# Performance work log

Hardware: AMD Instinct MI355X
Metric: run time of the kernel (lower is better)

Reference implementation:

```python
import jax, jax.numpy as jnp
import numpy as np

B, C, P, H, W, S = 4, 256, 128, 56, 56, 5
EPS = 1e-5


def setup_inputs() -> dict:
    key = jax.random.key(0)
    ks = jax.random.split(key, 6)
    return {
        "x": jax.random.normal(ks[0], (B, C, H, W), jnp.float32),
        "Wt": jax.random.normal(ks[1], (P, C), jnp.float32) * 0.05,
        "Wp": jax.random.normal(ks[2], (P, C), jnp.float32) * 0.05,
        "Wg": jax.random.normal(ks[3], (S, P, C), jnp.float32) * 0.05,
        "W1": jax.random.normal(ks[4], (S, C, P), jnp.float32) * 0.05,
        "W2": jax.random.normal(ks[5], (S, C, P), jnp.float32) * 0.05,
        "gamma": jnp.ones((S, C), jnp.float32),
        "beta": jnp.zeros((S, C), jnp.float32),
    }


def _batchnorm(o, g, b):
    # training-mode BN over (batch, spatial); o: [b, C, n]
    mean = o.mean(axis=(0, 2), keepdims=True)
    var = ((o - mean) ** 2).mean(axis=(0, 2), keepdims=True)
    return (o - mean) * jax.lax.rsqrt(var + EPS) * g[None, :, None] + b[None, :, None]


def reference(x, Wt, Wp, Wg, W1, W2, gamma, beta):
    b, c, h, w = x.shape
    n = h * w
    xf = x.reshape(b, c, n)
    # 1x1 conv projections == channel matmuls
    t = jax.nn.relu(jnp.einsum('pc,bcn->bpn', Wt, xf))  # is_norm branch uses relu
    p = jax.nn.relu(jnp.einsum('pc,bcn->bpn', Wp, xf))
    att = jnp.einsum('bpi,bpj->bij', t, p)              # [b, n, n] affinity
    att = 0.5 * (att + jnp.swapaxes(att, 1, 2))         # is_sys symmetrization
    d = att.sum(axis=2)                                  # degree [b, n]
    d_safe = jnp.where(d != 0, d, 1.0)
    d_inv = jnp.where(d != 0, jax.lax.rsqrt(d_safe), 0.0)
    att = att * d_inv[:, None, :] * d_inv[:, :, None]    # D^-1/2 A D^-1/2
    out = xf
    for s in range(S):  # fixed small stage count
        g = jnp.einsum('pc,bcn->bpn', Wg[s], out)        # [b, P, n]
        ag = jnp.einsum('bij,bpj->bpi', att, g)          # att @ g over spatial
        o = jnp.einsum('cp,bpn->bcn', W1[s], ag) + jnp.einsum('cp,bpn->bcn', W2[s], g)
        out = _batchnorm(o, gamma[s], beta[s]) + out     # BN + residual
    return out.reshape(b, c, h, w)
```

## Files before the change

kernel.cpp:

```cpp
#include <hip/hip_runtime.h>

namespace {

constexpr int Bc = 4;
constexpr int Cc = 256;
constexpr int Pc = 128;
constexpr int NcT = 3136;
constexpr int Np = 3200;
constexpr int Sc = 5;
constexpr int KSn = 5;
constexpr int KCH = 640;
constexpr float EPSc = 1e-5f;

typedef __attribute__((ext_vector_type(8))) short bf16x8;
typedef __attribute__((ext_vector_type(4))) float f32x4;
typedef __attribute__((ext_vector_type(8))) unsigned short u16x8;
typedef __attribute__((ext_vector_type(4))) unsigned short u16x4;

__device__ inline float bf2f(unsigned short u) {
    return __uint_as_float(((unsigned)u) << 16);
}
__device__ inline unsigned short f2bf(float f) {
    unsigned u = __float_as_uint(f);
    return (unsigned short)((u + 0x7FFFu + ((u >> 16) & 1u)) >> 16);
}

struct GP {
    const unsigned short* A; int lda; long aB; long aSl;
    const unsigned short* Bw; int ldb; long bB; long bSl;
    const unsigned short* A2; int lda2; long aB2;
    const unsigned short* B2; int ldb2; long bB2;
    int K; int K2; int nsl; int kchunk;
    unsigned short* outSM; int ldsm; long smB; long smSlice;
    unsigned short* outCM; long cmB;
    float* ps; float* ps2;
    const float* dinv;
    const unsigned short* oin; const float* bnsc; const float* bnsh;
    float* resid;
};

template <int MT, int EPI, int CMOUT, bool SPLITK, int BNSTAT, bool FUSEBN,
          bool XORM, bool DUALK>
__global__ __launch_bounds__(256) void mgemm(GP p)
{
    constexpr int TBA = MT * 64 * 2;
    constexpr int TBB = 128 * 64 * 2;
    constexpr int BUF = TBA + TBB;
    constexpr int OTB = MT * 132 * 4;
    constexpr int LDSZ = (2 * BUF > OTB + 2048) ? 2 * BUF : (OTB + 2048);
    __shared__ __align__(16) char lds[LDSZ];

    int b, kstart;
    long smOff;
    if (SPLITK) {
        b = blockIdx.z & 3;
        int ks = blockIdx.z >> 2;
        kstart = ks * p.kchunk;
        smOff = (long)ks * p.smSlice;
    } else {
        b = blockIdx.z; kstart = 0; smOff = 0;
    }
    const int n0 = blockIdx.x * 128;
    const int m0 = blockIdx.y * MT;
    const int tid = threadIdx.x;
    const int w = tid >> 6, l = tid & 63;

    const unsigned short* Ab = p.A + (size_t)b * p.aB + (size_t)m0 * p.lda;
    const unsigned short* Bb = p.Bw + (size_t)b * p.bB + (size_t)n0 * p.ldb;

    const int srow8 = tid >> 3;
    const int sgran = tid & 7;
    const int sswz = (sgran ^ (srow8 & 7)) * 8;
    constexpr int AR = MT / 32;

    constexpr int WC = (MT == 128) ? 2 : 4;
    constexpr int NB = 128 / WC / 16;
    const int wr = w / WC, wc = w % WC;

    f32x4 acc[4][NB] = {};
    float fup[AR][8];

    auto stage1 = [&](int buf, int sl, int k0) {
        char* base = lds + buf * BUF;
        const unsigned short* As = Ab + (size_t)sl * p.aSl + k0 + sswz;
#pragma unroll
        for (int j = 0; j < AR; ++j)
            __builtin_amdgcn_global_load_lds(
                (const __attribute__((address_space(1))) void*)
                    (As + (size_t)(j * 32 + srow8) * p.lda),
                (__attribute__((address_space(3))) void*)(base + j * 4096 + tid * 16),
                16, 0, 0);
        const unsigned short* Bs = Bb + (size_t)sl * p.bSl + k0 + sswz;
#pragma unroll
        for (int j = 0; j < 4; ++j)
            __builtin_amdgcn_global_load_lds(
                (const __attribute__((address_space(1))) void*)
                    (Bs + (size_t)(j * 32 + srow8) * p.ldb),
                (__attribute__((address_space(3))) void*)(base + TBA + j * 4096 + tid * 16),
                16, 0, 0);
    };

    auto stageB1 = [&](int buf, int k0) {
        char* base = lds + buf * BUF + TBA;
        const unsigned short* Bs = Bb + k0 + sswz;
#pragma unroll
        for (int j = 0; j < 4; ++j)
            __builtin_amdgcn_global_load_lds(
                (const __attribute__((address_space(1))) void*)
                    (Bs + (size_t)(j * 32 + srow8) * p.ldb),
                (__attribute__((address_space(3))) void*)(base + j * 4096 + tid * 16),
                16, 0, 0);
    };

    auto fbLoad = [&](int k0) {
        const float* scp = p.bnsc + k0 + sgran * 8;
        const float* shp = p.bnsh + k0 + sgran * 8;
        float4 s0 = *(const float4*)scp, s1 = *(const float4*)(scp + 4);
        float4 h0 = *(const float4*)shp, h1 = *(const float4*)(shp + 4);
#pragma unroll
        for (int j = 0; j < AR; ++j) {
            int row = j * 32 + srow8;
            int n = m0 + row;
            size_t off = ((size_t)b * Np + n) * 256 + k0 + sgran * 8;
            if (n < NcT) {
                u16x8 ov = *(const u16x8*)(p.oin + off);
                float4 r0 = *(const float4*)(p.resid + off);
                float4 r1 = *(const float4*)(p.resid + off + 4);
                fup[j][0] = r0.x + fmaf(bf2f(ov[0]), s0.x, h0.x);
                fup[j][1] = r0.y + fmaf(bf2f(ov[1]), s0.y, h0.y);
                fup[j][2] = r0.z + fmaf(bf2f(ov[2]), s0.z, h0.z);
                fup[j][3] = r0.w + fmaf(bf2f(ov[3]), s0.w, h0.w);
                fup[j][4] = r1.x + fmaf(bf2f(ov[4]), s1.x, h1.x);
                fup[j][5] = r1.y + fmaf(bf2f(ov[5]), s1.y, h1.y);
                fup[j][6] = r1.z + fmaf(bf2f(ov[6]), s1.z, h1.z);
                fup[j][7] = r1.w + fmaf(bf2f(ov[7]), s1.w, h1.w);
                float4 w0, w1;
                w0.x = fup[j][0]; w0.y = fup[j][1]; w0.z = fup[j][2]; w0.w = fup[j][3];
                w1.x = fup[j][4]; w1.y = fup[j][5]; w1.z = fup[j][6]; w1.w = fup[j][7];
                *(float4*)(p.resid + off) = w0;
                *(float4*)(p.resid + off + 4) = w1;
            } else {
#pragma unroll
                for (int i = 0; i < 8; ++i) fup[j][i] = 0.f;
            }
        }
    };
    auto fbWrite = [&](int buf) {
        char* base = lds + buf * BUF;
#pragma unroll
        for (int j = 0; j < AR; ++j) {
            int row = j * 32 + srow8;
            u16x8 hv;
#pragma unroll
            for (int i = 0; i < 8; ++i) hv[i] = f2bf(fup[j][i]);
            *(u16x8*)(base + row * 128 + ((sgran ^ (row & 7)) << 4)) = hv;
        }
    };

    auto compute = [&](int buf) {
        const char* base = lds + buf * BUF;
        const int lo = l & 15, gq = l >> 4;
#pragma unroll
        for (int kh = 0; kh < 2; ++kh) {
            const int lg = kh * 4 + gq;
            bf16x8 bf[NB];
#pragma unroll
            for (int c = 0; c < NB; ++c) {
                int brow = wc * (16 * NB) + c * 16 + lo;
                bf[c] = *(const bf16x8*)(base + TBA + brow * 128 +
                                         ((lg ^ (brow & 7)) << 4));
            }
#pragma unroll
            for (int r = 0; r < 4; ++r) {
                int arow = wr * 64 + r * 16 + lo;
                bf16x8 af = *(const bf16x8*)(base + arow * 128 +
                                             ((lg ^ (arow & 7)) << 4));
#pragma unroll
                for (int c = 0; c < NB; ++c)
                    acc[r][c] = __builtin_amdgcn_mfma_f32_16x16x32_bf16(
                        af, bf[c], acc[r][c], 0, 0, 0);
            }
        }
    };

    if constexpr (FUSEBN) {
        const int nst = p.K >> 6;
        fbLoad(kstart);
        fbWrite(0);
        stageB1(0, kstart);
        __syncthreads();
        for (int s = 0; s < nst; ++s) {
            if (s + 1 < nst) {
                fbLoad(kstart + ((s + 1) << 6));
                stageB1((s + 1) & 1, kstart + ((s + 1) << 6));
            }
            compute(s & 1);
            if (s + 1 < nst) fbWrite((s + 1) & 1);
            __syncthreads();
        }
    } else {
        const int nsteps1 = (SPLITK ? p.kchunk : p.K) >> 6;
        const int spl2 = DUALK ? (p.K2 >> 6) : 0;
        const int tot = p.nsl * nsteps1 + spl2;

        const unsigned short* Ab2 = DUALK ?
            (p.A2 + (size_t)b * p.aB2 + (size_t)m0 * p.lda2) : nullptr;
        const unsigned short* Bb2 = DUALK ?
            (p.B2 + (size_t)b * p.bB2 + (size_t)n0 * p.ldb2) : nullptr;
        auto stage2 = [&](int buf, int k0) {
            if constexpr (DUALK) {
                char* base = lds + buf * BUF;
                const unsigned short* As = Ab2 + k0 + sswz;
#pragma unroll
                for (int j = 0; j < AR; ++j)
                    __builtin_amdgcn_global_load_lds(
                        (const __attribute__((address_space(1))) void*)
                            (As + (size_t)(j * 32 + srow8) * p.lda2),
                        (__attribute__((address_space(3))) void*)(base + j * 4096 + tid * 16),
                        16, 0, 0);
                const unsigned short* Bs = Bb2 + k0 + sswz;
#pragma unroll
                for (int j = 0; j < 4; ++j)
                    __builtin_amdgcn_global_load_lds(
                        (const __attribute__((address_space(1))) void*)
                            (Bs + (size_t)(j * 32 + srow8) * p.ldb2),
                        (__attribute__((address_space(3))) void*)(base + TBA + j * 4096 + tid * 16),
                        16, 0, 0);
            }
        };

        stage1(0, 0, kstart);
        __syncthreads();
        int sl = 0, st = 1;
        if (st == nsteps1) { st = 0; sl = 1; }
        for (int gs = 0; gs < tot; ++gs) {
            if (gs + 1 < tot) {
                if (sl < p.nsl) stage1((gs + 1) & 1, sl, kstart + (st << 6));
                else            stage2((gs + 1) & 1, st << 6);
                ++st;
                int lim = (sl < p.nsl) ? nsteps1 : spl2;
                if (st == lim) { st = 0; ++sl; }
            }
            compute(gs & 1);
            __syncthreads();
        }
    }

    float* ot = (float*)lds;
    {
        const int lo = l & 15, gq = l >> 4;
#pragma unroll
        for (int r = 0; r < 4; ++r)
#pragma unroll
            for (int c = 0; c < NB; ++c)
#pragma unroll
                for (int j = 0; j < 4; ++j) {
                    float v = acc[r][c][j];
                    if (EPI == 1) v = fmaxf(v, 0.f);
                    ot[(wr * 64 + r * 16 + gq * 4 + j) * 132 +
                       wc * (16 * NB) + c * 16 + lo] = v;
                }
    }
    __syncthreads();

    {
        constexpr int TPR = 256 / MT;
        const int r = tid / TPR;
        const int c0 = (tid % TPR) * (MT / 2);
        const int m0s = XORM ? (m0 ^ 128) : m0;
        unsigned short* dst = p.outSM + (size_t)b * p.smB + smOff +
                              (size_t)(m0s + r) * p.ldsm + n0 + c0;
#pragma unroll
        for (int k = 0; k < MT / 16; ++k) {
            u16x8 o;
#pragma unroll
            for (int j = 0; j < 8; ++j) o[j] = f2bf(ot[r * 132 + c0 + 8 * k + j]);
            *(u16x8*)(dst + 8 * k) = o;
        }
    }

    if (CMOUT) {
        const int c = tid >> 1, r0 = (tid & 1) * (MT / 2);
        const float* dv = p.dinv + (size_t)b * Np + m0 + r0;
        unsigned short* dst = p.outCM + (size_t)b * p.cmB +
                              (size_t)(n0 + c) * Np + m0 + r0;
#pragma unroll
        for (int k = 0; k < MT / 16; ++k) {
            u16x8 o;
#pragma unroll
            for (int j = 0; j < 8; ++j) {
                float v = ot[(r0 + 8 * k + j) * 132 + c];
                if (CMOUT == 2) v *= dv[8 * k + j];
                o[j] = f2bf(v);
            }
            *(u16x8*)(dst + 8 * k) = o;
        }
    }

    if (BNSTAT) {
        float* p1 = (float*)(lds + OTB);
        float* p2 = p1 + 256;
        const int col = tid & 127, half = tid >> 7;
        float s = 0.f, s2 = 0.f;
#pragma unroll
        for (int i = 0; i < MT / 2; ++i) {
            float v = ot[(half * (MT / 2) + i) * 132 + col];
            s += v;
            if (BNSTAT == 2) s2 = fmaf(v, v, s2);
        }
        p1[half * 128 + col] = s;
        if (BNSTAT == 2) p2[half * 128 + col] = s2;
        __syncthreads();
        if (tid < 128) {
            float aa = p1[tid] + p1[128 + tid];
            size_t slot = ((size_t)b * gridDim.y + blockIdx.y) * 256 + n0 + tid;
            p.ps[slot] = aa;
            if (BNSTAT == 2) p.ps2[slot] = p2[tid] + p2[128 + tid];
        }
    }
}

__global__ __launch_bounds__(256) void prep_k(
    const float* __restrict__ x, const float* __restrict__ Wt,
    const float* __restrict__ Wp, const float* __restrict__ Wg,
    const float* __restrict__ W1, const float* __restrict__ W2,
    unsigned short* __restrict__ Wcomb, unsigned short* __restrict__ Wgh,
    unsigned short* __restrict__ W1h, unsigned short* __restrict__ W2h,
    float* __restrict__ out_sm, unsigned short* __restrict__ outh)
{
    __shared__ float tb[64][65];
    int item = blockIdx.x;
    int t = threadIdx.x;
    if (item < 544) {
        size_t e = ((size_t)item * 256 + t) * 4;
        const float* src; unsigned short* dst;
        if (e < 32768)       { src = Wt + e;           dst = Wcomb + e; }
        else if (e < 65536)  { src = Wp + (e - 32768); dst = Wcomb + e; }
        else if (e < 229376) { size_t o = e - 65536;  src = Wg + o; dst = Wgh + o; }
        else if (e < 393216) { size_t o = e - 229376; src = W1 + o; dst = W1h + o; }
        else                 { size_t o = e - 393216; src = W2 + o; dst = W2h + o; }
        float4 v = *(const float4*)src;
        u16x4 t4;
        t4[0] = f2bf(v.x); t4[1] = f2bf(v.y); t4[2] = f2bf(v.z); t4[3] = f2bf(v.w);
        *(u16x4*)dst = t4;
        return;
    }
    int it = item - 544;
    int nx = it % 50, cy = (it / 50) % 4, b = it / 200;
    int c0 = cy * 64, n0 = nx * 64;
    const bool pad = (n0 >= NcT);
    if (!pad) {
        int ci = t >> 2, nb = (t & 3) * 16;
        const float* src = x + ((size_t)b * Cc + c0 + ci) * NcT + n0 + nb;
#pragma unroll
        for (int k = 0; k < 4; ++k) {
            float4 v = *(const float4*)(src + 4 * k);
            tb[ci][nb + 4 * k + 0] = v.x; tb[ci][nb + 4 * k + 1] = v.y;
            tb[ci][nb + 4 * k + 2] = v.z; tb[ci][nb + 4 * k + 3] = v.w;
        }
    }
    __syncthreads();
    int r = t >> 2, cb = (t & 3) * 16;
    size_t off = ((size_t)b * Np + n0 + r) * 256 + c0 + cb;
    float vv[16];
#pragma unroll
    for (int j = 0; j < 16; ++j) vv[j] = pad ? 0.f : tb[cb + j][r];
    float* dst = out_sm + off;
#pragma unroll
    for (int k = 0; k < 4; ++k) {
        float4 v; v.x = vv[4*k]; v.y = vv[4*k+1]; v.z = vv[4*k+2]; v.w = vv[4*k+3];
        *(float4*)(dst + 4 * k) = v;
    }
    u16x8 h1, h2;
#pragma unroll
    for (int j = 0; j < 8; ++j) { h1[j] = f2bf(vv[j]); h2[j] = f2bf(vv[8 + j]); }
    unsigned short* dh = outh + off;
    *(u16x8*)dh = h1;
    *(u16x8*)(dh + 8) = h2;
}

__global__ __launch_bounds__(256) void dinv_k(
    const unsigned short* __restrict__ U, const float* __restrict__ rp,
    float* __restrict__ dinv)
{
    __shared__ float rsl[256];
    int b = blockIdx.y, tid = threadIdx.x;
    float s = 0.f;
    for (int j = 0; j < 25; ++j) s += rp[((size_t)b * 25 + j) * 256 + tid];
    rsl[tid ^ 128] = s;
    __syncthreads();
    int i = blockIdx.x * 256 + tid;
    if (i < Np) {
        const unsigned short* row = U + ((size_t)b * Np + i) * 256;
        float acc = 0.f;
        for (int q0 = 0; q0 < 256; q0 += 8) {
            u16x8 v = *(const u16x8*)(row + q0);
#pragma unroll
            for (int j = 0; j < 8; ++j) acc = fmaf(bf2f(v[j]), rsl[q0 + j], acc);
        }
        float d = 0.5f * acc;
        dinv[(size_t)b * Np + i] = d > 0.f ? rsqrtf(d) : 0.f;
    }
}

__global__ __launch_bounds__(256) void ud_k(
    const unsigned short* __restrict__ U, const float* __restrict__ dinv,
    unsigned short* __restrict__ Ud)
{
    size_t e = ((size_t)blockIdx.x * 256 + threadIdx.x) * 8;
    float sc = 0.5f * dinv[e >> 8];
    u16x8 v = *(const u16x8*)(U + e);
    u16x8 o;
#pragma unroll
    for (int j = 0; j < 8; ++j) o[j] = f2bf(bf2f(v[j]) * sc);
    *(u16x8*)(Ud + e) = o;
}

__global__ __launch_bounds__(256) void bnfin_k(
    const float* __restrict__ ps, const float* __restrict__ ps2,
    const float* __restrict__ gamma, const float* __restrict__ beta,
    float* __restrict__ scale, float* __restrict__ shift)
{
    __shared__ float l1[256], l2[256];
    int t = threadIdx.x;
    int c = blockIdx.x * 16 + (t & 15);
    int gl = t >> 4;
    float a = 0.f, a2 = 0.f;
    for (int g = gl; g < 100; g += 16) {
        a += ps[(size_t)g * 256 + c];
        a2 += ps2[(size_t)g * 256 + c];
    }
    l1[t] = a; l2[t] = a2;
    __syncthreads();
    if (gl == 0) {
#pragma unroll
        for (int j = 1; j < 16; ++j) {
            a += l1[j * 16 + (t & 15)];
            a2 += l2[j * 16 + (t & 15)];
        }
        const float inv = 1.f / (float)(Bc * NcT);
        float mean = a * inv;
        float var = a2 * inv - mean * mean;
        float sc = gamma[c] * rsqrtf(var + EPSc);
        scale[c] = sc;
        shift[c] = beta[c] - mean * sc;
    }
}

__global__ __launch_bounds__(256) void xpoutbn_k(
    const float* __restrict__ out_sm, const unsigned short* __restrict__ oin,
    const float* __restrict__ scale, const float* __restrict__ shift,
    float* __restrict__ outp)
{
    __shared__ float tb[64][65];
    __shared__ float lsc[64], lsh[64];
    int b = blockIdx.z, c0 = blockIdx.y * 64, n0 = blockIdx.x * 64;
    int t = threadIdx.x;
    if (t < 64) { lsc[t] = scale[c0 + t]; lsh[t] = shift[c0 + t]; }
    __syncthreads();
    {
        int r = t >> 2, cb = (t & 3) * 16;
        size_t off = ((size_t)b * Np + n0 + r) * 256 + c0 + cb;
#pragma unroll
        for (int k = 0; k < 2; ++k) {
            float4 a0 = *(const float4*)(out_sm + off + 8 * k);
            float4 a1 = *(const float4*)(out_sm + off + 8 * k + 4);
            u16x8 ov = *(const u16x8*)(oin + off + 8 * k);
            tb[r][cb + 8*k + 0] = a0.x + fmaf(bf2f(ov[0]), lsc[cb + 8*k + 0], lsh[cb + 8*k + 0]);
            tb[r][cb + 8*k + 1] = a0.y + fmaf(bf2f(ov[1]), lsc[cb + 8*k + 1], lsh[cb + 8*k + 1]);
            tb[r][cb + 8*k + 2] = a0.z + fmaf(bf2f(ov[2]), lsc[cb + 8*k + 2], lsh[cb + 8*k + 2]);
            tb[r][cb + 8*k + 3] = a0.w + fmaf(bf2f(ov[3]), lsc[cb + 8*k + 3], lsh[cb + 8*k + 3]);
            tb[r][cb + 8*k + 4] = a1.x + fmaf(bf2f(ov[4]), lsc[cb + 8*k + 4], lsh[cb + 8*k + 4]);
            tb[r][cb + 8*k + 5] = a1.y + fmaf(bf2f(ov[5]), lsc[cb + 8*k + 5], lsh[cb + 8*k + 5]);
            tb[r][cb + 8*k + 6] = a1.z + fmaf(bf2f(ov[6]), lsc[cb + 8*k + 6], lsh[cb + 8*k + 6]);
            tb[r][cb + 8*k + 7] = a1.w + fmaf(bf2f(ov[7]), lsc[cb + 8*k + 7], lsh[cb + 8*k + 7]);
        }
    }
    __syncthreads();
    {
        int c = t >> 2, rb = (t & 3) * 16;
        float vv[16];
#pragma unroll
        for (int j = 0; j < 16; ++j) vv[j] = tb[rb + j][c];
        float* dst = outp + ((size_t)b * Cc + c0 + c) * NcT + n0 + rb;
#pragma unroll
        for (int k = 0; k < 4; ++k) {
            float4 v; v.x = vv[4*k]; v.y = vv[4*k+1]; v.z = vv[4*k+2]; v.w = vv[4*k+3];
            *(float4*)(dst + 4 * k) = v;
        }
    }
}

}

extern "C" void kernel_launch(void* const* d_in, const int* in_sizes, int n_in,
                              void* d_out, int out_size, void* d_ws, size_t ws_size,
                              hipStream_t stream) {
    const float* x     = (const float*)d_in[0];
    const float* Wt    = (const float*)d_in[1];
    const float* Wp    = (const float*)d_in[2];
    const float* Wg    = (const float*)d_in[3];
    const float* W1    = (const float*)d_in[4];
    const float* W2    = (const float*)d_in[5];
    const float* gamma = (const float*)d_in[6];
    const float* beta  = (const float*)d_in[7];

    char* p = (char*)d_ws;
    auto alloc = [&](size_t bytes) { char* r = p; p += (bytes + 255) & ~(size_t)255; return r; };
    float*          out_sm = (float*)         alloc((size_t)Bc * Np * 256 * 4);
    unsigned short* outh   = (unsigned short*)alloc((size_t)Bc * Np * 256 * 2);
    unsigned short* U_sm   = (unsigned short*)alloc((size_t)Bc * Np * 256 * 2);
    unsigned short* U_cm   = (unsigned short*)alloc((size_t)Bc * 256 * Np * 2);
    unsigned short* Ud     = (unsigned short*)alloc((size_t)Bc * Np * 256 * 2);
    unsigned short* g_sm   = (unsigned short*)alloc((size_t)Bc * Np * Pc * 2);
    unsigned short* g_cmd  = (unsigned short*)alloc((size_t)Bc * Pc * Np * 2);
    unsigned short* o_sm   = (unsigned short*)alloc((size_t)Bc * Np * 256 * 2);
    unsigned short* Cpart  = (unsigned short*)alloc((size_t)KSn * Bc * 256 * Pc * 2);
    unsigned short* WMb    = (unsigned short*)alloc((size_t)Bc * Cc * 256 * 2);
    unsigned short* Wcomb  = (unsigned short*)alloc((size_t)Cc * Cc * 2);
    unsigned short* Wgh    = (unsigned short*)alloc((size_t)Sc * Pc * Cc * 2);
    unsigned short* W1h    = (unsigned short*)alloc((size_t)Sc * Cc * Pc * 2);
    unsigned short* W2h    = (unsigned short*)alloc((size_t)Sc * Cc * Pc * 2);
    float*          rp     = (float*)         alloc((size_t)100 * 256 * 4);
    float*          dinv   = (float*)         alloc((size_t)Bc * Np * 4);
    float*          ps     = (float*)         alloc((size_t)100 * 256 * 4);
    float*          ps2    = (float*)         alloc((size_t)100 * 256 * 4);
    float*          scale  = (float*)         alloc(256 * 4);
    float*          shiftb = (float*)         alloc(256 * 4);

    const long NpC = (long)Np * 256;
    dim3 blk(256);

    prep_k<<<1344, blk, 0, stream>>>(x, Wt, Wp, Wg, W1, W2,
                                     Wcomb, Wgh, W1h, W2h, out_sm, outh);

    {
        GP g{};
        g.A = outh; g.lda = 256; g.aB = NpC; g.aSl = 0;
        g.Bw = Wcomb; g.ldb = 256; g.bB = 0; g.bSl = 0;
        g.K = 256; g.nsl = 1;
        g.outSM = U_sm; g.ldsm = 256; g.smB = NpC; g.smSlice = 0;
        g.outCM = U_cm; g.cmB = (long)256 * Np;
        g.ps = rp;
        mgemm<128, 1, 1, false, 1, false, false, false>
            <<<dim3(2, 25, Bc), blk, 0, stream>>>(g);
    }

    dinv_k<<<dim3(13, Bc), blk, 0, stream>>>(U_sm, rp, dinv);
    ud_k<<<1600, blk, 0, stream>>>(U_sm, dinv, Ud);

    for (int s = 0; s < Sc; ++s) {
        {
            GP g{};
            g.A = outh; g.lda = 256; g.aB = NpC; g.aSl = 0;
            g.Bw = Wgh + (size_t)s * Pc * Cc; g.ldb = 256; g.bB = 0; g.bSl = 0;
            g.K = 256; g.nsl = 1;
            g.outSM = g_sm; g.ldsm = 128; g.smB = (long)Np * 128; g.smSlice = 0;
            g.outCM = g_cmd; g.cmB = (long)Pc * Np;
            g.dinv = dinv;
            g.oin = o_sm; g.bnsc = scale; g.bnsh = shiftb; g.resid = out_sm;
            if (s == 0)
                mgemm<64, 0, 2, false, 0, false, false, false>
                    <<<dim3(1, 50, Bc), blk, 0, stream>>>(g);
            else
                mgemm<64, 0, 2, false, 0, true, false, false>
                    <<<dim3(1, 50, Bc), blk, 0, stream>>>(g);
        }
        {
            GP g{};
            g.A = U_cm; g.lda = Np; g.aB = (long)256 * Np; g.aSl = 0;
            g.Bw = g_cmd; g.ldb = Np; g.bB = (long)Pc * Np; g.bSl = 0;
            g.K = Np; g.kchunk = KCH; g.nsl = 1;
            g.outSM = Cpart; g.ldsm = 128; g.smB = (long)256 * Pc;
            g.smSlice = (long)Bc * 256 * Pc;
            mgemm<64, 0, 0, true, 0, false, true, false>
                <<<dim3(1, 4, KSn * Bc), blk, 0, stream>>>(g);
        }
        {
            GP g{};
            g.A = W1h + (size_t)s * Cc * Pc; g.lda = 128; g.aB = 0; g.aSl = 0;
            g.Bw = Cpart; g.ldb = 128; g.bB = (long)256 * Pc;
            g.bSl = (long)Bc * 256 * Pc;
            g.K = 128; g.nsl = KSn;
            g.outSM = WMb; g.ldsm = 256; g.smB = (long)Cc * 256; g.smSlice = 0;
            mgemm<64, 0, 0, false, 0, false, false, false>
                <<<dim3(2, 4, Bc), blk, 0, stream>>>(g);
        }
        {
            GP g{};
            g.A = Ud; g.lda = 256; g.aB = NpC; g.aSl = 0;
            g.Bw = WMb; g.ldb = 256; g.bB = (long)Cc * 256; g.bSl = 0;
            g.K = 256; g.nsl = 1;
            g.A2 = g_sm; g.lda2 = 128; g.aB2 = (long)Np * 128;
            g.B2 = W2h + (size_t)s * Cc * Pc; g.ldb2 = 128; g.bB2 = 0;
            g.K2 = 128;
            g.outSM = o_sm; g.ldsm = 256; g.smB = NpC; g.smSlice = 0;
            g.ps = ps; g.ps2 = ps2;
            mgemm<128, 0, 0, false, 2, false, false, true>
                <<<dim3(2, 25, Bc), blk, 0, stream>>>(g);
        }
        bnfin_k<<<16, blk, 0, stream>>>(ps, ps2, gamma + s * Cc, beta + s * Cc,
                                        scale, shiftb);
    }

    xpoutbn_k<<<dim3(49, 4, Bc), blk, 0, stream>>>(out_sm, o_sm, scale, shiftb,
                                                   (float*)d_out);
}
```

Baseline: 271.0 us.

## Deepen GEMM pipeline to 4-stage LDS buffering and fuse dinv with Ud scaling

The non-FUSEBN GEMM path goes from double buffering to a 4-buffer ring that prefetches three K-steps ahead. It waits with explicit vmcnt counts and a raw s_barrier in place of a full __syncthreads each step, so global-to-LDS loads overlap compute more deeply. Separately, the degree-inverse kernel and the Ud scaling kernel are merged into one launch that reuses the block's dinv values from LDS. The trade-offs are four times the LDS per block, which may cut occupancy, and only 52 blocks for the merged elementwise kernel instead of 1600.

```diff
diff --git a/kernel.cpp b/kernel.cpp
--- a/kernel.cpp
+++ b/kernel.cpp
@@ -1,4 +1,6 @@
 #include <hip/hip_runtime.h>
+
+#define VMC(n) asm volatile("s_waitcnt vmcnt(" #n ")" ::: "memory")
 
 namespace {
 
@@ -34,8 +36,9 @@
     unsigned short* outSM; int ldsm; long smB; long smSlice;
     unsigned short* outCM; long cmB;
     float* ps; float* ps2;
+    const float* bnsc; const float* bnsh;
     const float* dinv;
-    const unsigned short* oin; const float* bnsc; const float* bnsh;
+    const unsigned short* oin;
     float* resid;
 };
 
@@ -47,7 +50,7 @@
     constexpr int TBB = 128 * 64 * 2;
     constexpr int BUF = TBA + TBB;
     constexpr int OTB = MT * 132 * 4;
-    constexpr int LDSZ = (2 * BUF > OTB + 2048) ? 2 * BUF : (OTB + 2048);
+    constexpr int LDSZ = (4 * BUF > OTB + 2048) ? 4 * BUF : (OTB + 2048);
     __shared__ __align__(16) char lds[LDSZ];
 
     int b, kstart;
@@ -201,7 +204,8 @@
     } else {
         const int nsteps1 = (SPLITK ? p.kchunk : p.K) >> 6;
         const int spl2 = DUALK ? (p.K2 >> 6) : 0;
-        const int tot = p.nsl * nsteps1 + spl2;
+        const int loop1 = p.nsl * nsteps1;
+        const int tot = loop1 + spl2;
 
         const unsigned short* Ab2 = DUALK ?
             (p.A2 + (size_t)b * p.aB2 + (size_t)m0 * p.lda2) : nullptr;
@@ -229,21 +233,35 @@
             }
         };
 
-        stage1(0, 0, kstart);
+        auto stage_g = [&](int buf, int g) {
+            if (g < loop1) {
+                int sl = g / nsteps1;
+                int st = g - sl * nsteps1;
+                stage1(buf, sl, kstart + (st << 6));
+            } else {
+                stage2(buf, (g - loop1) << 6);
+            }
+        };
+
+        stage_g(0, 0);
+        if (1 < tot) stage_g(1, 1);
+        if (2 < tot) stage_g(2, 2);
+        for (int gs = 0; gs < tot; ++gs) {
+            if constexpr (MT == 64) {
+                if (gs + 2 < tot) VMC(12);
+                else if (gs + 1 < tot) VMC(6);
+                else VMC(0);
+            } else {
+                if (gs + 2 < tot) VMC(16);
+                else if (gs + 1 < tot) VMC(8);
+                else VMC(0);
+            }
+            __builtin_amdgcn_s_barrier();
+            __builtin_amdgcn_sched_barrier(0);
+            if (gs + 3 < tot) stage_g((gs + 3) & 3, gs + 3);
+            compute(gs & 3);
+        }
         __syncthreads();
-        int sl = 0, st = 1;
-        if (st == nsteps1) { st = 0; sl = 1; }
-        for (int gs = 0; gs < tot; ++gs) {
-            if (gs + 1 < tot) {
-                if (sl < p.nsl) stage1((gs + 1) & 1, sl, kstart + (st << 6));
-                else            stage2((gs + 1) & 1, st << 6);
-                ++st;
-                int lim = (sl < p.nsl) ? nsteps1 : spl2;
-                if (st == lim) { st = 0; ++sl; }
-            }
-            compute(gs & 1);
-            __syncthreads();
-        }
     }
 
     float* ot = (float*)lds;
@@ -379,17 +397,20 @@
     *(u16x8*)(dh + 8) = h2;
 }
 
-__global__ __launch_bounds__(256) void dinv_k(
+__global__ __launch_bounds__(256) void dinvud_k(
     const unsigned short* __restrict__ U, const float* __restrict__ rp,
-    float* __restrict__ dinv)
+    float* __restrict__ dinv, unsigned short* __restrict__ Ud)
 {
     __shared__ float rsl[256];
+    __shared__ float dl[256];
     int b = blockIdx.y, tid = threadIdx.x;
     float s = 0.f;
     for (int j = 0; j < 25; ++j) s += rp[((size_t)b * 25 + j) * 256 + tid];
     rsl[tid ^ 128] = s;
     __syncthreads();
-    int i = blockIdx.x * 256 + tid;
+    const int i0 = blockIdx.x * 256;
+    const int i = i0 + tid;
+    float dv = 0.f;
     if (i < Np) {
         const unsigned short* row = U + ((size_t)b * Np + i) * 256;
         float acc = 0.f;
@@ -399,21 +420,24 @@
             for (int j = 0; j < 8; ++j) acc = fmaf(bf2f(v[j]), rsl[q0 + j], acc);
         }
         float d = 0.5f * acc;
-        dinv[(size_t)b * Np + i] = d > 0.f ? rsqrtf(d) : 0.f;
-    }
-}
-
-__global__ __launch_bounds__(256) void ud_k(
-    const unsigned short* __restrict__ U, const float* __restrict__ dinv,
-    unsigned short* __restrict__ Ud)
-{
-    size_t e = ((size_t)blockIdx.x * 256 + threadIdx.x) * 8;
-    float sc = 0.5f * dinv[e >> 8];
-    u16x8 v = *(const u16x8*)(U + e);
-    u16x8 o;
-#pragma unroll
-    for (int j = 0; j < 8; ++j) o[j] = f2bf(bf2f(v[j]) * sc);
-    *(u16x8*)(Ud + e) = o;
+        dv = d > 0.f ? rsqrtf(d) : 0.f;
+        dinv[(size_t)b * Np + i] = dv;
+    }
+    dl[tid] = 0.5f * dv;
+    __syncthreads();
+    for (int pass = 0; pass < 32; ++pass) {
+        int row = pass * 8 + (tid >> 5);
+        int gi = i0 + row;
+        if (gi < Np) {
+            size_t off = ((size_t)b * Np + gi) * 256 + (tid & 31) * 8;
+            u16x8 v = *(const u16x8*)(U + off);
+            float sc = dl[row];
+            u16x8 o;
+#pragma unroll
+            for (int j = 0; j < 8; ++j) o[j] = f2bf(bf2f(v[j]) * sc);
+            *(u16x8*)(Ud + off) = o;
+        }
+    }
 }
 
 __global__ __launch_bounds__(256) void bnfin_k(
@@ -546,8 +570,7 @@
             <<<dim3(2, 25, Bc), blk, 0, stream>>>(g);
     }
 
-    dinv_k<<<dim3(13, Bc), blk, 0, stream>>>(U_sm, rp, dinv);
-    ud_k<<<1600, blk, 0, stream>>>(U_sm, dinv, Ud);
+    dinvud_k<<<dim3(13, Bc), blk, 0, stream>>>(U_sm, rp, dinv, Ud);
 
     for (int s = 0; s < Sc; ++s) {
         {
```

Result: faster. 256.9 us (-5.2%).
